# Optimization experiments

Measured on AMD Instinct MI355X. Metric: run time of the kernel, lower is better.

The kernel has to match this reference:

```python
import jax, jax.numpy as jnp
import numpy as np

E_DIM = 64
N_EMBED = 8192

def setup_inputs() -> dict:
    key = jax.random.key(0)
    k1, k2 = jax.random.split(key)
    x = jax.random.normal(k1, (16, E_DIM, 32, 32), dtype=jnp.float32)   # [B, e_dim, H, W]
    embed = jax.random.normal(k2, (E_DIM, N_EMBED), dtype=jnp.float32)  # codebook [e_dim, n_embed]
    return {"x": x, "embed": embed}

def reference(x, embed):
    e_dim, n_embed = embed.shape
    # NCHW -> NHWC
    xp = jnp.transpose(x, (0, 2, 3, 1))              # [B, H, W, e_dim]
    flat = xp.reshape(-1, e_dim)                     # [N, e_dim]
    # squared-distance expansion: ||f||^2 - 2 f.E + ||e||^2  -> [N, n_embed]
    distance = (jnp.sum(flat * flat, axis=1, keepdims=True)
                - 2.0 * flat @ embed
                + jnp.sum(embed * embed, axis=0, keepdims=True))
    embed_idx = jnp.argmax(-distance, axis=1)        # [N] nearest code ids
    embed_idx = embed_idx.reshape(xp.shape[:-1])     # [B, H, W]
    # gather codes: embedding table is embed.T -> [n_embed, e_dim]
    quantize = jnp.take(embed.T, embed_idx, axis=0)  # [B, H, W, e_dim]
    return quantize
```

## Files before the change

### kernel.cpp

```cpp
#include <hip/hip_runtime.h>


typedef __attribute__((ext_vector_type(8))) __bf16 bf16x8;
typedef __attribute__((ext_vector_type(4))) float f32x4;
typedef unsigned int u32;
typedef unsigned long long u64;

union frag_cast { f32x4 f; bf16x8 b; };
__device__ __forceinline__ bf16x8 as_bf16x8(f32x4 v) { frag_cast u; u.f = v; return u.b; }

#define N_ROWS  16384
#define E_DIM   64
#define N_EMBED 8192
#define NCHUNK  16
#define COLS_PER_BLOCK (N_EMBED / NCHUNK)
#define N_ST (COLS_PER_BLOCK / 64)
#define ROWS_PER_BLOCK 256
#define N_ROWBLK (N_ROWS / ROWS_PER_BLOCK)
#define NT 4
#define MARGIN_THR 2e-3f

#define WS_AH   0u
#define WS_AL   (2u << 20)
#define WS_B    (4u << 20)
#define WS_ET   (6u << 20)
#define WS_BIAS (8u << 20)
#define WS_PB1  (WS_BIAS + (64u << 10))
#define WS_PI1  (WS_PB1 + (1u << 20))
#define WS_PB2  (WS_PI1 + (1u << 20))
#define WS_FIDX (WS_PB2 + (1u << 20))
#define WS_FLAG (WS_FIDX + (64u << 10))
#define WS_CNT  (WS_FLAG + (64u << 10))
#define WS_FKEY (WS_CNT + (4u << 10))

__device__ __forceinline__ u32 f32_key(float s) {
    u32 u = __float_as_uint(s);
    return (u & 0x80000000u) ? ~u : (u | 0x80000000u);
}

__device__ __forceinline__ void async16(const void* g, void* l) {
    __builtin_amdgcn_global_load_lds(
        (const __attribute__((address_space(1))) void*)g,
        (__attribute__((address_space(3))) void*)l, 16, 0, 0);
}

__global__ __launch_bounds__(256) void prep(
        const float* __restrict__ x, const float* __restrict__ embed, char* ws) {
    __shared__ float tile[64][65];
    __bf16* Ah = (__bf16*)(ws + WS_AH);
    __bf16* Al = (__bf16*)(ws + WS_AL);
    float*  eT = (float*)(ws + WS_ET);
    float*  bias = (float*)(ws + WS_BIAS);
    const int t = threadIdx.x;
    const int blk = blockIdx.x;

    if (blk < 256) {
        const int b = blk >> 4, p0 = (blk & 15) * 64;
        {
            const int c = t >> 2, seg = (t & 3) * 16;
            const float* src = x + b * 65536 + c * 1024 + p0 + seg;
#pragma unroll
            for (int i = 0; i < 16; ++i) tile[c][seg + i] = src[i];
        }
        __syncthreads();
        const int p = t >> 2, cq = (t & 3) * 16;
        const long row = b * 1024 + p0 + p;
        bf16x8 vh0, vh1, vl0, vl1;
#pragma unroll
        for (int i = 0; i < 16; ++i) {
            float f = tile[cq + i][p];
            __bf16 h = (__bf16)f;
            __bf16 l = (__bf16)(f - (float)h);
            if (i < 8) { vh0[i] = h; vl0[i] = l; }
            else       { vh1[i - 8] = h; vl1[i - 8] = l; }
        }
        *(bf16x8*)(Ah + row * 64 + cq) = vh0;
        *(bf16x8*)(Ah + row * 64 + cq + 8) = vh1;
        *(bf16x8*)(Al + row * 64 + cq) = vl0;
        *(bf16x8*)(Al + row * 64 + cq + 8) = vl1;
    } else {
        if (blk == 256 && t == 0) *(int*)(ws + WS_CNT) = 0;
        const int g = blk - 256;
        const int jbase = g * 64;
        char* Bg = ws + WS_B + (size_t)g * 16384;
        {
            const int c = t >> 2, seg = (t & 3) * 16;
            const float* src = embed + c * N_EMBED + jbase + seg;
#pragma unroll
            for (int i = 0; i < 16; ++i) tile[c][seg + i] = src[i];
        }
        __syncthreads();
        if (t < 64) {
            float s = 0.f;
#pragma unroll
            for (int c = 0; c < 64; ++c) { float v = tile[c][t]; s = fmaf(v, v, s); }
            bias[jbase + t] = -0.5f * s;
        }
        const int jl = t >> 2, cq = (t & 3) * 16;
        bf16x8 vh0, vh1, vl0, vl1;
#pragma unroll
        for (int i = 0; i < 16; ++i) {
            float f = tile[cq + i][jl];
            eT[(long)(jbase + jl) * 64 + cq + i] = f;
            __bf16 h = (__bf16)f;
            __bf16 l = (__bf16)(f - (float)h);
            if (i < 8) { vh0[i] = h; vl0[i] = l; }
            else       { vh1[i - 8] = h; vl1[i - 8] = l; }
        }
        const int k0 = (cq >> 3), sw = jl & 7;
        __bf16* hi = (__bf16*)Bg + jl * 64;
        __bf16* lo = (__bf16*)(Bg + 8192) + jl * 64;
        *(bf16x8*)(hi + ((k0 ^ sw) * 8))       = vh0;
        *(bf16x8*)(hi + (((k0 + 1) ^ sw) * 8)) = vh1;
        *(bf16x8*)(lo + ((k0 ^ sw) * 8))       = vl0;
        *(bf16x8*)(lo + (((k0 + 1) ^ sw) * 8)) = vl1;
    }
}

__global__ __launch_bounds__(256, 4) void qdist(const char* __restrict__ ws_c, char* __restrict__ ws) {
    __shared__ __align__(16) char smem[2][16384];
    const __bf16* Ah = (const __bf16*)(ws_c + WS_AH);
    const __bf16* Al = (const __bf16*)(ws_c + WS_AL);
    const char* Bws = ws_c + WS_B;
    const float* biasg = (const float*)(ws_c + WS_BIAS);
    float* pb1 = (float*)(ws + WS_PB1);
    int*   pi1 = (int*)(ws + WS_PI1);
    float* pb2 = (float*)(ws + WS_PB2);

    const int t = threadIdx.x;
    const int wv = t >> 6, lane = t & 63, ln = lane & 15, q = lane >> 4;
    const int rb = blockIdx.x >> 4, chunk = blockIdx.x & 15;
    const int row0 = rb * ROWS_PER_BLOCK;
    const int col0 = chunk * COLS_PER_BLOCK;
    const int g0 = col0 >> 6;

    f32x4 pfh[NT][2], pfl[NT][2];
#pragma unroll
    for (int nt = 0; nt < NT; ++nt) {
        long row = row0 + wv * 64 + nt * 16 + ln;
        long base = row * 64 + q * 8;
        pfh[nt][0] = *(const f32x4*)(Ah + base);
        pfh[nt][1] = *(const f32x4*)(Ah + base + 32);
        pfl[nt][0] = *(const f32x4*)(Al + base);
        pfl[nt][1] = *(const f32x4*)(Al + base + 32);
    }
    asm volatile("" :
        "+v"(pfh[0][0]), "+v"(pfh[0][1]), "+v"(pfh[1][0]), "+v"(pfh[1][1]),
        "+v"(pfh[2][0]), "+v"(pfh[2][1]), "+v"(pfh[3][0]), "+v"(pfh[3][1]),
        "+v"(pfl[0][0]), "+v"(pfl[0][1]), "+v"(pfl[1][0]), "+v"(pfl[1][1]),
        "+v"(pfl[2][0]), "+v"(pfl[2][1]), "+v"(pfl[3][0]), "+v"(pfl[3][1]));

    float b1[NT], b2[NT]; int iq[NT];
#pragma unroll
    for (int k = 0; k < NT; ++k) { b1[k] = -3.4e38f; b2[k] = -3.4e38f; iq[k] = 0; }

    const int s7 = ln & 7;
    const int rdbase = ln * 128 + ((q ^ s7) << 4);

    auto issue = [&](int st) {
        const char* src = Bws + (size_t)(g0 + st) * 16384;
        char* dst = smem[st & 1];
#pragma unroll
        for (int s = 0; s < 4; ++s)
            async16(src + s * 4096 + wv * 1024 + lane * 16,
                    dst + s * 4096 + wv * 1024);
    };

    issue(0);
    for (int st = 0; st < N_ST; ++st) {
        __syncthreads();
        if (st + 1 < N_ST) issue(st + 1);
        const char* buf = smem[st & 1];
        __builtin_amdgcn_s_setprio(1);
#pragma unroll
        for (int ct = 0; ct < 4; ++ct) {
            const int boff = ct * 2048 + rdbase;
            bf16x8 ah0 = *(const bf16x8*)(buf + boff);
            bf16x8 ah1 = *(const bf16x8*)(buf + (boff ^ 64));
            bf16x8 al0 = *(const bf16x8*)(buf + 8192 + boff);
            bf16x8 al1 = *(const bf16x8*)(buf + 8192 + (boff ^ 64));
            const int cbase = col0 + st * 64 + ct * 16;
            f32x4 bv = *(const f32x4*)(biasg + cbase + q * 4);
            const int jq = cbase + q * 4;
#pragma unroll
            for (int nt = 0; nt < NT; ++nt) {
                f32x4 acc = __builtin_amdgcn_mfma_f32_16x16x32_bf16(al0, as_bf16x8(pfh[nt][0]), bv, 0, 0, 0);
                acc = __builtin_amdgcn_mfma_f32_16x16x32_bf16(al1, as_bf16x8(pfh[nt][1]), acc, 0, 0, 0);
                acc = __builtin_amdgcn_mfma_f32_16x16x32_bf16(ah0, as_bf16x8(pfl[nt][0]), acc, 0, 0, 0);
                acc = __builtin_amdgcn_mfma_f32_16x16x32_bf16(ah1, as_bf16x8(pfl[nt][1]), acc, 0, 0, 0);
                acc = __builtin_amdgcn_mfma_f32_16x16x32_bf16(ah0, as_bf16x8(pfh[nt][0]), acc, 0, 0, 0);
                acc = __builtin_amdgcn_mfma_f32_16x16x32_bf16(ah1, as_bf16x8(pfh[nt][1]), acc, 0, 0, 0);
                float mx = fmaxf(fmaxf(acc[0], acc[1]), fmaxf(acc[2], acc[3]));
                b2[nt] = fmaxf(b2[nt], fminf(b1[nt], mx));
                bool gt = mx > b1[nt];
                b1[nt] = fmaxf(b1[nt], mx);
                iq[nt] = gt ? jq : iq[nt];
            }
        }
        __builtin_amdgcn_s_setprio(0);
    }

#pragma unroll
    for (int m = 16; m < 64; m <<= 1) {
#pragma unroll
        for (int nt = 0; nt < NT; ++nt) {
            float o1 = __shfl_xor(b1[nt], m);
            int   oi = __shfl_xor(iq[nt], m);
            float o2 = __shfl_xor(b2[nt], m);
            b2[nt] = fmaxf(fmaxf(fminf(b1[nt], o1), o2), b2[nt]);
            bool take = (o1 > b1[nt]) || (o1 == b1[nt] && oi < iq[nt]);
            if (take) { b1[nt] = o1; iq[nt] = oi; }
        }
    }
    if (q == 0) {
#pragma unroll
        for (int nt = 0; nt < NT; ++nt) {
            int pixel = row0 + wv * 64 + nt * 16 + ln;
            int o = chunk * N_ROWS + pixel;
            pb1[o] = b1[nt];
            pi1[o] = iq[nt];
            pb2[o] = b2[nt];
        }
    }
}

__global__ __launch_bounds__(64) void reduce_rows(const float* __restrict__ x, char* ws) {
    const float* pb1 = (const float*)(ws + WS_PB1);
    const int*   pi1 = (const int*)(ws + WS_PI1);
    const float* pb2 = (const float*)(ws + WS_PB2);
    const float* eT = (const float*)(ws + WS_ET);
    const float* bias = (const float*)(ws + WS_BIAS);
    int* fidx = (int*)(ws + WS_FIDX);
    int* flags = (int*)(ws + WS_FLAG);
    int* cnt = (int*)(ws + WS_CNT);
    u64* fkey = (u64*)(ws + WS_FKEY);
    const int row = blockIdx.x * 64 + threadIdx.x;

    float b1 = pb1[row]; int iq = pi1[row]; float b2 = pb2[row];
#pragma unroll
    for (int ch = 1; ch < NCHUNK; ++ch) {
        float o1 = pb1[ch * N_ROWS + row];
        int   oi = pi1[ch * N_ROWS + row];
        float o2 = pb2[ch * N_ROWS + row];
        b2 = fmaxf(fmaxf(fminf(b1, o1), o2), b2);
        if (o1 > b1 || (o1 == b1 && oi < iq)) { b1 = o1; iq = oi; }
    }

    if (b1 - b2 < MARGIN_THR) {
        fidx[row] = -1;
        fkey[row] = 0ull;
        flags[atomicAdd(cnt, 1)] = row;
    } else {
        float xr[64];
        const float* xb = x + (row >> 10) * 65536 + (row & 1023);
#pragma unroll
        for (int c = 0; c < 64; ++c) xr[c] = xb[c * 1024];
        float best = -3.4e38f; int bi = iq;
#pragma unroll
        for (int cc = 0; cc < 4; ++cc) {
            const int j = iq + cc;
            const float* e = eT + j * 64;
            float s = bias[j];
#pragma unroll
            for (int c = 0; c < 64; ++c) s = fmaf(xr[c], e[c], s);
            if (s > best) { best = s; bi = j; }
        }
        fidx[row] = bi;
    }
}

__global__ __launch_bounds__(256) void recheck(const float* __restrict__ x, char* ws) {
    __shared__ float fl[64];
    __shared__ u64 red[256];
    const float* eT = (const float*)(ws + WS_ET);
    const float* bias = (const float*)(ws + WS_BIAS);
    const int* flags = (const int*)(ws + WS_FLAG);
    const int n = *(const int*)(ws + WS_CNT);
    u64* fkey = (u64*)(ws + WS_FKEY);
    const int t = threadIdx.x;
    const int seg = blockIdx.x & 31;
    const int rstep = gridDim.x >> 5;
    const int j = seg * 256 + t;

    for (int rowi = blockIdx.x >> 5; rowi < n; rowi += rstep) {
        const int row = flags[rowi];
        __syncthreads();
        if (t < 64) fl[t] = x[(row >> 10) * 65536 + t * 1024 + (row & 1023)];
        __syncthreads();
        float xr[64];
#pragma unroll
        for (int c = 0; c < 64; ++c) xr[c] = fl[c];

        const f32x4* e = (const f32x4*)(eT + (size_t)j * 64);
        f32x4 a0 = {0.f, 0.f, 0.f, 0.f}, a1 = a0, a2 = a0, a3 = a0;
#pragma unroll
        for (int v = 0; v < 4; ++v) {
            f32x4 e0 = e[v * 4 + 0], e1 = e[v * 4 + 1];
            f32x4 e2 = e[v * 4 + 2], e3 = e[v * 4 + 3];
#pragma unroll
            for (int k = 0; k < 4; ++k) {
                a0[k] = fmaf(xr[v * 16 + k],      e0[k], a0[k]);
                a1[k] = fmaf(xr[v * 16 + 4 + k],  e1[k], a1[k]);
                a2[k] = fmaf(xr[v * 16 + 8 + k],  e2[k], a2[k]);
                a3[k] = fmaf(xr[v * 16 + 12 + k], e3[k], a3[k]);
            }
        }
        f32x4 a01 = a0 + a1, a23 = a2 + a3;
        f32x4 as = a01 + a23;
        float s = bias[j] + ((as[0] + as[1]) + (as[2] + as[3]));

        red[t] = ((u64)f32_key(s) << 32) | (u32)(~(u32)j);
        __syncthreads();
        for (int off = 128; off; off >>= 1) {
            if (t < off) { u64 o = red[t + off]; if (o > red[t]) red[t] = o; }
            __syncthreads();
        }
        if (t == 0) atomicMax(&fkey[row], red[0]);
        __syncthreads();
    }
}

__global__ __launch_bounds__(256) void gather_out(const char* __restrict__ ws,
                                                  float* __restrict__ out) {
    const int* fidx = (const int*)(ws + WS_FIDX);
    const u64* fkey = (const u64*)(ws + WS_FKEY);
    const float* eT = (const float*)(ws + WS_ET);
    int g = blockIdx.x * 256 + threadIdx.x;
    int row = g >> 6, c = g & 63;
    int idx = fidx[row];
    if (idx < 0) idx = (int)(~(u32)(fkey[row] & 0xffffffffull));
    out[g] = eT[idx * 64 + c];
}

extern "C" void kernel_launch(void* const* d_in, const int* in_sizes, int n_in,
                              void* d_out, int out_size, void* d_ws, size_t ws_size,
                              hipStream_t stream) {
    const float* x     = (const float*)d_in[0];
    const float* embed = (const float*)d_in[1];
    float* out = (float*)d_out;
    char* ws = (char*)d_ws;

    prep<<<384, 256, 0, stream>>>(x, embed, ws);
    qdist<<<N_ROWBLK * NCHUNK, 256, 0, stream>>>(ws, ws);
    reduce_rows<<<N_ROWS / 64, 64, 0, stream>>>(x, ws);
    recheck<<<2048, 256, 0, stream>>>(x, ws);
    gather_out<<<(N_ROWS * 64) / 256, 256, 0, stream>>>(ws, out);
}
```

Before: 132.5 us.

## Fuse row reduction and gather into qdist and recheck via last-block atomics

```diff
diff --git a/kernel.cpp b/kernel.cpp
--- a/kernel.cpp
+++ b/kernel.cpp
@@ -15,9 +15,9 @@
 #define NCHUNK  16
 #define COLS_PER_BLOCK (N_EMBED / NCHUNK)
 #define N_ST (COLS_PER_BLOCK / 64)
-#define ROWS_PER_BLOCK 256
+#define ROWS_PER_BLOCK 512
 #define N_ROWBLK (N_ROWS / ROWS_PER_BLOCK)
-#define NT 4
+#define NT 8
 #define MARGIN_THR 2e-3f
 
 #define WS_AH   0u
@@ -25,13 +25,14 @@
 #define WS_B    (4u << 20)
 #define WS_ET   (6u << 20)
 #define WS_BIAS (8u << 20)
-#define WS_PB1  (WS_BIAS + (64u << 10))
+#define WS_CNT  (WS_BIAS + (32u << 10))
+#define WS_ARR  (WS_CNT + 64u)
+#define WS_PB1  (WS_CNT + (4u << 10))
 #define WS_PI1  (WS_PB1 + (1u << 20))
 #define WS_PB2  (WS_PI1 + (1u << 20))
-#define WS_FIDX (WS_PB2 + (1u << 20))
-#define WS_FLAG (WS_FIDX + (64u << 10))
-#define WS_CNT  (WS_FLAG + (64u << 10))
-#define WS_FKEY (WS_CNT + (4u << 10))
+#define WS_FLAG (WS_PB2 + (1u << 20))
+#define WS_FKEY (WS_FLAG + (64u << 10))
+#define WS_DONE (WS_FKEY + (128u << 10))
 
 __device__ __forceinline__ u32 f32_key(float s) {
     u32 u = __float_as_uint(s);
@@ -79,7 +80,10 @@
         *(bf16x8*)(Al + row * 64 + cq) = vl0;
         *(bf16x8*)(Al + row * 64 + cq + 8) = vl1;
     } else {
-        if (blk == 256 && t == 0) *(int*)(ws + WS_CNT) = 0;
+        if (blk == 256) {
+            if (t == 0) *(int*)(ws + WS_CNT) = 0;
+            if (t < 32) ((int*)(ws + WS_ARR))[t] = 0;
+        }
         const int g = blk - 256;
         const int jbase = g * 64;
         char* Bg = ws + WS_B + (size_t)g * 16384;
@@ -117,8 +121,11 @@
     }
 }
 
-__global__ __launch_bounds__(256, 4) void qdist(const char* __restrict__ ws_c, char* __restrict__ ws) {
+__global__ __launch_bounds__(256, 2) void qdist(const char* __restrict__ ws_c, char* ws,
+                                                const float* __restrict__ x,
+                                                float* __restrict__ out) {
     __shared__ __align__(16) char smem[2][16384];
+    __shared__ int isLast;
     const __bf16* Ah = (const __bf16*)(ws_c + WS_AH);
     const __bf16* Al = (const __bf16*)(ws_c + WS_AL);
     const char* Bws = ws_c + WS_B;
@@ -137,7 +144,7 @@
     f32x4 pfh[NT][2], pfl[NT][2];
 #pragma unroll
     for (int nt = 0; nt < NT; ++nt) {
-        long row = row0 + wv * 64 + nt * 16 + ln;
+        long row = row0 + wv * 128 + nt * 16 + ln;
         long base = row * 64 + q * 8;
         pfh[nt][0] = *(const f32x4*)(Ah + base);
         pfh[nt][1] = *(const f32x4*)(Ah + base + 32);
@@ -147,8 +154,13 @@
     asm volatile("" :
         "+v"(pfh[0][0]), "+v"(pfh[0][1]), "+v"(pfh[1][0]), "+v"(pfh[1][1]),
         "+v"(pfh[2][0]), "+v"(pfh[2][1]), "+v"(pfh[3][0]), "+v"(pfh[3][1]),
+        "+v"(pfh[4][0]), "+v"(pfh[4][1]), "+v"(pfh[5][0]), "+v"(pfh[5][1]),
+        "+v"(pfh[6][0]), "+v"(pfh[6][1]), "+v"(pfh[7][0]), "+v"(pfh[7][1]));
+    asm volatile("" :
         "+v"(pfl[0][0]), "+v"(pfl[0][1]), "+v"(pfl[1][0]), "+v"(pfl[1][1]),
-        "+v"(pfl[2][0]), "+v"(pfl[2][1]), "+v"(pfl[3][0]), "+v"(pfl[3][1]));
+        "+v"(pfl[2][0]), "+v"(pfl[2][1]), "+v"(pfl[3][0]), "+v"(pfl[3][1]),
+        "+v"(pfl[4][0]), "+v"(pfl[4][1]), "+v"(pfl[5][0]), "+v"(pfl[5][1]),
+        "+v"(pfl[6][0]), "+v"(pfl[6][1]), "+v"(pfl[7][0]), "+v"(pfl[7][1]));
 
     float b1[NT], b2[NT]; int iq[NT];
 #pragma unroll
@@ -215,75 +227,87 @@
     if (q == 0) {
 #pragma unroll
         for (int nt = 0; nt < NT; ++nt) {
-            int pixel = row0 + wv * 64 + nt * 16 + ln;
+            int pixel = row0 + wv * 128 + nt * 16 + ln;
             int o = chunk * N_ROWS + pixel;
             pb1[o] = b1[nt];
             pi1[o] = iq[nt];
             pb2[o] = b2[nt];
         }
     }
-}
-
-__global__ __launch_bounds__(64) void reduce_rows(const float* __restrict__ x, char* ws) {
-    const float* pb1 = (const float*)(ws + WS_PB1);
-    const int*   pi1 = (const int*)(ws + WS_PI1);
-    const float* pb2 = (const float*)(ws + WS_PB2);
-    const float* eT = (const float*)(ws + WS_ET);
-    const float* bias = (const float*)(ws + WS_BIAS);
-    int* fidx = (int*)(ws + WS_FIDX);
+
+    __threadfence();
+    if (t == 0)
+        isLast = (atomicAdd((int*)(ws + WS_ARR) + rb, 1) == NCHUNK - 1) ? 1 : 0;
+    __syncthreads();
+    if (!isLast) return;
+    __threadfence();
+
+    const float* eT = (const float*)(ws_c + WS_ET);
     int* flags = (int*)(ws + WS_FLAG);
     int* cnt = (int*)(ws + WS_CNT);
     u64* fkey = (u64*)(ws + WS_FKEY);
-    const int row = blockIdx.x * 64 + threadIdx.x;
-
-    float b1 = pb1[row]; int iq = pi1[row]; float b2 = pb2[row];
-#pragma unroll
-    for (int ch = 1; ch < NCHUNK; ++ch) {
-        float o1 = pb1[ch * N_ROWS + row];
-        int   oi = pi1[ch * N_ROWS + row];
-        float o2 = pb2[ch * N_ROWS + row];
-        b2 = fmaxf(fmaxf(fminf(b1, o1), o2), b2);
-        if (o1 > b1 || (o1 == b1 && oi < iq)) { b1 = o1; iq = oi; }
-    }
-
-    if (b1 - b2 < MARGIN_THR) {
-        fidx[row] = -1;
-        fkey[row] = 0ull;
-        flags[atomicAdd(cnt, 1)] = row;
-    } else {
-        float xr[64];
-        const float* xb = x + (row >> 10) * 65536 + (row & 1023);
-#pragma unroll
-        for (int c = 0; c < 64; ++c) xr[c] = xb[c * 1024];
-        float best = -3.4e38f; int bi = iq;
-#pragma unroll
-        for (int cc = 0; cc < 4; ++cc) {
-            const int j = iq + cc;
-            const float* e = eT + j * 64;
-            float s = bias[j];
-#pragma unroll
-            for (int c = 0; c < 64; ++c) s = fmaf(xr[c], e[c], s);
-            if (s > best) { best = s; bi = j; }
-        }
-        fidx[row] = bi;
-    }
-}
-
-__global__ __launch_bounds__(256) void recheck(const float* __restrict__ x, char* ws) {
+    int* done = (int*)(ws + WS_DONE);
+
+#pragma unroll
+    for (int rr = 0; rr < 2; ++rr) {
+        const int row = row0 + rr * 256 + t;
+        float m1 = pb1[row]; int mi = pi1[row]; float m2 = pb2[row];
+#pragma unroll
+        for (int ch = 1; ch < NCHUNK; ++ch) {
+            float o1 = pb1[ch * N_ROWS + row];
+            int   oi = pi1[ch * N_ROWS + row];
+            float o2 = pb2[ch * N_ROWS + row];
+            m2 = fmaxf(fmaxf(fminf(m1, o1), o2), m2);
+            if (o1 > m1 || (o1 == m1 && oi < mi)) { m1 = o1; mi = oi; }
+        }
+        if (m1 - m2 < MARGIN_THR) {
+            fkey[row] = 0ull;
+            done[row] = 0;
+            flags[atomicAdd(cnt, 1)] = row;
+        } else {
+            const float* xb = x + (row >> 10) * 65536 + (row & 1023);
+            const float* e0 = eT + (size_t)mi * 64;
+            const float* e1 = e0 + 64;
+            const float* e2 = e0 + 128;
+            const float* e3 = e0 + 192;
+            const float* bb = (const float*)(ws_c + WS_BIAS) + mi;
+            float s0 = bb[0], s1 = bb[1], s2 = bb[2], s3 = bb[3];
+#pragma unroll
+            for (int c = 0; c < 64; ++c) {
+                float xc = xb[c * 1024];
+                s0 = fmaf(xc, e0[c], s0);
+                s1 = fmaf(xc, e1[c], s1);
+                s2 = fmaf(xc, e2[c], s2);
+                s3 = fmaf(xc, e3[c], s3);
+            }
+            int bi = mi; float best = s0;
+            if (s1 > best) { best = s1; bi = mi + 1; }
+            if (s2 > best) { best = s2; bi = mi + 2; }
+            if (s3 > best) { best = s3; bi = mi + 3; }
+            const f32x4* src = (const f32x4*)(eT + (size_t)bi * 64);
+            f32x4* dst = (f32x4*)(out + (size_t)row * 64);
+#pragma unroll
+            for (int v = 0; v < 16; ++v) dst[v] = src[v];
+        }
+    }
+}
+
+__global__ __launch_bounds__(256) void recheck(const float* __restrict__ x, char* ws,
+                                               float* __restrict__ out) {
     __shared__ float fl[64];
     __shared__ u64 red[256];
+    __shared__ int sLast, sIdx;
     const float* eT = (const float*)(ws + WS_ET);
     const float* bias = (const float*)(ws + WS_BIAS);
     const int* flags = (const int*)(ws + WS_FLAG);
     const int n = *(const int*)(ws + WS_CNT);
     u64* fkey = (u64*)(ws + WS_FKEY);
+    int* done = (int*)(ws + WS_DONE);
     const int t = threadIdx.x;
-    const int seg = blockIdx.x & 31;
-    const int rstep = gridDim.x >> 5;
-    const int j = seg * 256 + t;
-
-    for (int rowi = blockIdx.x >> 5; rowi < n; rowi += rstep) {
-        const int row = flags[rowi];
+
+    for (int e = blockIdx.x; e < n * 32; e += gridDim.x) {
+        const int row = flags[e >> 5];
+        const int seg = e & 31;
         __syncthreads();
         if (t < 64) fl[t] = x[(row >> 10) * 65536 + t * 1024 + (row & 1023)];
         __syncthreads();
@@ -291,12 +315,13 @@
 #pragma unroll
         for (int c = 0; c < 64; ++c) xr[c] = fl[c];
 
-        const f32x4* e = (const f32x4*)(eT + (size_t)j * 64);
+        const int j = seg * 256 + t;
+        const f32x4* ecd = (const f32x4*)(eT + (size_t)j * 64);
         f32x4 a0 = {0.f, 0.f, 0.f, 0.f}, a1 = a0, a2 = a0, a3 = a0;
 #pragma unroll
         for (int v = 0; v < 4; ++v) {
-            f32x4 e0 = e[v * 4 + 0], e1 = e[v * 4 + 1];
-            f32x4 e2 = e[v * 4 + 2], e3 = e[v * 4 + 3];
+            f32x4 e0 = ecd[v * 4 + 0], e1 = ecd[v * 4 + 1];
+            f32x4 e2 = ecd[v * 4 + 2], e3 = ecd[v * 4 + 3];
 #pragma unroll
             for (int k = 0; k < 4; ++k) {
                 a0[k] = fmaf(xr[v * 16 + k],      e0[k], a0[k]);
@@ -315,21 +340,22 @@
             if (t < off) { u64 o = red[t + off]; if (o > red[t]) red[t] = o; }
             __syncthreads();
         }
-        if (t == 0) atomicMax(&fkey[row], red[0]);
-        __syncthreads();
-    }
-}
-
-__global__ __launch_bounds__(256) void gather_out(const char* __restrict__ ws,
-                                                  float* __restrict__ out) {
-    const int* fidx = (const int*)(ws + WS_FIDX);
-    const u64* fkey = (const u64*)(ws + WS_FKEY);
-    const float* eT = (const float*)(ws + WS_ET);
-    int g = blockIdx.x * 256 + threadIdx.x;
-    int row = g >> 6, c = g & 63;
-    int idx = fidx[row];
-    if (idx < 0) idx = (int)(~(u32)(fkey[row] & 0xffffffffull));
-    out[g] = eT[idx * 64 + c];
+        if (t == 0) {
+            atomicMax(&fkey[row], red[0]);
+            __threadfence();
+            sLast = (atomicAdd(&done[row], 1) == 31) ? 1 : 0;
+        }
+        __syncthreads();
+        if (sLast) {
+            if (t == 0) {
+                u64 k = atomicMax(&fkey[row], 0ull);
+                sIdx = (int)(~(u32)(k & 0xffffffffull));
+            }
+            __syncthreads();
+            if (t < 64) out[(size_t)row * 64 + t] = eT[(size_t)sIdx * 64 + t];
+        }
+        __syncthreads();
+    }
 }
 
 extern "C" void kernel_launch(void* const* d_in, const int* in_sizes, int n_in,
@@ -341,8 +367,6 @@
     char* ws = (char*)d_ws;
 
     prep<<<384, 256, 0, stream>>>(x, embed, ws);
-    qdist<<<N_ROWBLK * NCHUNK, 256, 0, stream>>>(ws, ws);
-    reduce_rows<<<N_ROWS / 64, 64, 0, stream>>>(x, ws);
-    recheck<<<2048, 256, 0, stream>>>(x, ws);
-    gather_out<<<(N_ROWS * 64) / 256, 256, 0, stream>>>(ws, out);
-}
+    qdist<<<N_ROWBLK * NCHUNK, 256, 0, stream>>>(ws, ws, x, out);
+    recheck<<<2048, 256, 0, stream>>>(x, ws, out);
+}
```

After: 250.5 us. 1.89x slower.
